# Kernel tuning notes

Hardware: AMD Instinct MI355X
Metric: run time of the kernel (lower is better)

Reference implementation:

```python
import jax, jax.numpy as jnp
import numpy as np

N = 100000   # nodes
E = 1600000  # edges
F_IN = 128
H = 128
C_OUT = 10
G = 128      # graphs in batch
EPS = 1e-5


def setup_inputs() -> dict:
    key = jax.random.key(0)
    ks = jax.random.split(key, 16)
    x = jax.random.normal(ks[0], (N, F_IN), dtype=jnp.float32)
    edge_index = jax.random.randint(ks[1], (2, E), 0, N, dtype=jnp.int64)
    batch = jnp.sort(jax.random.randint(ks[2], (N,), 0, G, dtype=jnp.int64))
    s = 1.0 / np.sqrt(H)
    inp = {"x": x, "edge_index": edge_index, "batch": batch}
    # GCNConv weights/biases
    inp["w1"] = jax.random.normal(ks[3], (F_IN, H), jnp.float32) * s
    inp["b1"] = jax.random.normal(ks[4], (H,), jnp.float32) * 0.01
    inp["w2"] = jax.random.normal(ks[5], (H, H), jnp.float32) * s
    inp["b2"] = jax.random.normal(ks[6], (H,), jnp.float32) * 0.01
    inp["w3"] = jax.random.normal(ks[7], (H, H), jnp.float32) * s
    inp["b3"] = jax.random.normal(ks[8], (H,), jnp.float32) * 0.01
    # GraphNorm params: scale (weight), shift (bias), mean_scale (alpha)
    for i, k in zip((1, 2, 3), (ks[9], ks[10], ks[11])):
        kk = jax.random.split(k, 3)
        inp[f"g{i}w"] = 1.0 + 0.1 * jax.random.normal(kk[0], (H,), jnp.float32)
        inp[f"g{i}b"] = 0.1 * jax.random.normal(kk[1], (H,), jnp.float32)
        inp[f"g{i}a"] = 1.0 + 0.1 * jax.random.normal(kk[2], (H,), jnp.float32)
    inp["lw"] = jax.random.normal(ks[12], (H, C_OUT), jnp.float32) * s
    inp["lb"] = jax.random.normal(ks[13], (C_OUT,), jnp.float32) * 0.01
    return inp


def _gcn_norm(edge_index, n):
    # add self loops, symmetric normalization D^-1/2 (A+I) D^-1/2
    loop = jnp.arange(n, dtype=edge_index.dtype)
    src = jnp.concatenate([edge_index[0], loop])
    dst = jnp.concatenate([edge_index[1], loop])
    deg = jax.ops.segment_sum(jnp.ones_like(dst, dtype=jnp.float32), dst, num_segments=n)
    dinv = jnp.where(deg > 0, jax.lax.rsqrt(deg), 0.0)
    norm = dinv[src] * dinv[dst]
    return src, dst, norm


def _gcn_conv(x, w, b, src, dst, norm, n):
    h = x @ w                              # [N,H]
    msg = h[src] * norm[:, None]           # gather + edge weight
    out = jax.ops.segment_sum(msg, dst, num_segments=n)  # scatter-add
    return out + b


def _graph_norm(x, weight, bias, alpha, batch, cnt, g):
    mean = jax.ops.segment_sum(x, batch, num_segments=g) / cnt[:, None]
    sub = x - alpha * mean[batch]
    var = jax.ops.segment_sum(sub * sub, batch, num_segments=g) / cnt[:, None]
    return weight * sub * jax.lax.rsqrt(var[batch] + EPS) + bias


def reference(x, edge_index, batch, w1, b1, w2, b2, w3, b3,
              g1w, g1b, g1a, g2w, g2b, g2a, g3w, g3b, g3a, lw, lb):
    n = x.shape[0]
    src, dst, norm = _gcn_norm(edge_index, n)
    cnt = jnp.maximum(jax.ops.segment_sum(jnp.ones((n,), jnp.float32), batch, num_segments=G), 1.0)
    # dropout is identity in eval mode
    h = _gcn_conv(x, w1, b1, src, dst, norm, n)
    h = jax.nn.relu(_graph_norm(h, g1w, g1b, g1a, batch, cnt, G))
    h = _gcn_conv(h, w2, b2, src, dst, norm, n)
    h = jax.nn.relu(_graph_norm(h, g2w, g2b, g2a, batch, cnt, G))
    h = _gcn_conv(h, w3, b3, src, dst, norm, n)
    h = jax.nn.relu(_graph_norm(h, g3w, g3b, g3a, batch, cnt, G))
    pooled = jax.ops.segment_sum(h, batch, num_segments=G) / cnt[:, None]  # global_mean_pool
    logits = pooled @ lw + lb
    return jax.nn.log_softmax(logits, axis=1)
```

## Files before the change

### kernel.cpp

```cpp
#include <hip/hip_runtime.h>

#define NN 100000
#define NE 1600000
#define HD 128
#define NG 128
#define NC 10
#define EPSV 1e-5f

#define BSH 9
#define NBKT ((NN + 511) >> 9)
#define BIN_BLOCKS ((NE + 4095) / 4096)

typedef __attribute__((ext_vector_type(8))) short short8;
typedef __attribute__((ext_vector_type(4))) float f32x4;

__device__ __forceinline__ float b2f(ushort u){ return __uint_as_float(((unsigned)u)<<16); }
__device__ __forceinline__ ushort f2b(float f){
  unsigned u = __float_as_uint(f);
  unsigned r = (u + 0x7FFFu + ((u>>16)&1u)) >> 16;
  return (ushort)r;
}

__global__ __launch_bounds__(256)
void k_init(const int* __restrict__ batch, int* __restrict__ gstart,
            const float* __restrict__ w1, const float* __restrict__ w2,
            const float* __restrict__ w3, ushort* __restrict__ wT,
            int* __restrict__ gbhist, float* __restrict__ zero_base)
{
  int b = blockIdx.x, t = threadIdx.x;
  if(b < 391){
    int n = b*256 + t;
    if(n >= NN) return;
    int bb = batch[n];
    if(n == 0){
      for(int g=0; g<=bb; g++) gstart[g] = 0;
      int last = batch[NN-1];
      for(int g=last+1; g<=NG; g++) gstart[g] = NN;
    } else {
      int bp = batch[n-1];
      for(int g=bp+1; g<=bb; g++) gstart[g] = n;
    }
  } else if(b < 394){
    const float* w = (b == 391) ? w1 : (b == 392) ? w2 : w3;
    ushort* o = wT + (b-391)*16384;
    #pragma unroll 4
    for(int i=0;i<64;i++){
      int e = i*256 + t;
      int k = e>>7, h = e&127;
      o[h*128 + k] = f2b(w[e]);
    }
  } else if(b < 408){
    #pragma unroll 8
    for(int i=0;i<32;i++) zero_base[(size_t)(b-394)*8192 + i*256 + t] = 0.f;
  } else {
    if(t < NBKT) gbhist[t] = 0;
  }
}

__global__ __launch_bounds__(256) void k_bhist(const int* __restrict__ ei, int* __restrict__ gbhist){
  __shared__ int h[NBKT];
  int t = threadIdx.x;
  if(t < NBKT) h[t] = 0;
  __syncthreads();
  int base = blockIdx.x*4096;
  #pragma unroll
  for(int i=0;i<16;i++){
    int e = base + i*256 + t;
    if(e < NE) atomicAdd(&h[ei[NE + e] >> BSH], 1);
  }
  __syncthreads();
  if(t < NBKT && h[t]) atomicAdd(&gbhist[t], h[t]);
}

__global__ void k_bscan(const int* __restrict__ gbhist, int* __restrict__ bucket_base,
                        int* __restrict__ bucket_cursor, int* __restrict__ rowstart){
  __shared__ int lds[256];
  int t = threadIdx.x;
  int v = (t < NBKT) ? gbhist[t] : 0;
  lds[t] = v; __syncthreads();
  for(int off=1; off<256; off<<=1){
    int y = lds[t]; int z = (t>=off)?lds[t-off]:0;
    __syncthreads(); lds[t] = y+z; __syncthreads();
  }
  int excl = (t>0)?lds[t-1]:0;
  if(t < NBKT){ bucket_base[t] = excl; bucket_cursor[t] = excl; }
  if(t == 0){ bucket_base[NBKT] = NE; rowstart[NN] = NE; }
}

__global__ __launch_bounds__(256) void k_bin(const int* __restrict__ ei, int* __restrict__ bucket_cursor,
                                             unsigned* __restrict__ ebuf){
  __shared__ unsigned eb[4096];
  __shared__ unsigned char bb4[4096];
  __shared__ int hist[NBKT], lstart[NBKT], lcur[NBKT], rbase[NBKT];
  __shared__ int scanbuf[256];
  int t = threadIdx.x;
  if(t < NBKT) hist[t] = 0;
  __syncthreads();
  int base = blockIdx.x*4096;
  int nv = NE - base; if(nv > 4096) nv = 4096;
  int se[16], de[16];
  #pragma unroll
  for(int i=0;i<16;i++){
    int e = base + i*256 + t;
    if(e < NE){ se[i] = ei[e]; de[i] = ei[NE + e]; atomicAdd(&hist[de[i] >> BSH], 1); }
  }
  __syncthreads();
  int v = (t < NBKT) ? hist[t] : 0;
  scanbuf[t] = v; __syncthreads();
  for(int off=1; off<256; off<<=1){
    int y = scanbuf[t]; int z = (t>=off)?scanbuf[t-off]:0;
    __syncthreads(); scanbuf[t] = y+z; __syncthreads();
  }
  if(t < NBKT){
    int excl = (t>0)?scanbuf[t-1]:0;
    lstart[t] = excl; lcur[t] = excl;
    if(hist[t]) rbase[t] = atomicAdd(&bucket_cursor[t], hist[t]);
  }
  __syncthreads();
  #pragma unroll
  for(int i=0;i<16;i++){
    int e = base + i*256 + t;
    if(e < NE){
      int b = de[i] >> BSH;
      int idx = atomicAdd(&lcur[b], 1);
      eb[idx] = ((unsigned)(de[i] & 511) << 17) | (unsigned)se[i];
      bb4[idx] = (unsigned char)b;
    }
  }
  __syncthreads();
  #pragma unroll
  for(int i=0;i<16;i++){
    int slot = i*256 + t;
    if(slot < nv){
      int b = bb4[slot];
      ebuf[rbase[b] + (slot - lstart[b])] = eb[slot];
    }
  }
}

__global__ __launch_bounds__(256) void k_sort(const unsigned* __restrict__ ebuf,
                                              const int* __restrict__ bucket_base,
                                              int* __restrict__ srcs, int* __restrict__ rowstart,
                                              float* __restrict__ dinv){
  __shared__ int hist[512], cur[512];
  __shared__ int scanbuf[256];
  int b = blockIdx.x, t = threadIdx.x;
  int e0 = bucket_base[b], e1 = bucket_base[b+1];
  hist[t] = 0; hist[t+256] = 0;
  __syncthreads();
  for(int i = e0 + t; i < e1; i += 256){
    atomicAdd(&hist[ebuf[i] >> 17], 1);
  }
  __syncthreads();
  int s0 = hist[2*t], s1 = hist[2*t+1];
  scanbuf[t] = s0 + s1; __syncthreads();
  for(int off=1; off<256; off<<=1){
    int y = scanbuf[t]; int z = (t>=off)?scanbuf[t-off]:0;
    __syncthreads(); scanbuf[t] = y+z; __syncthreads();
  }
  int excl = (t>0)?scanbuf[t-1]:0;
  cur[2*t] = excl; cur[2*t+1] = excl + s0;
  int d0 = (b << BSH) + 2*t, d1 = d0 + 1;
  if(d0 < NN){ rowstart[d0] = e0 + excl;      dinv[d0] = rsqrtf((float)(s0 + 1)); }
  if(d1 < NN){ rowstart[d1] = e0 + excl + s0; dinv[d1] = rsqrtf((float)(s1 + 1)); }
  __syncthreads();
  for(int i = e0 + t; i < e1; i += 256){
    unsigned pk = ebuf[i];
    int dl = pk >> 17;
    int pos = e0 + atomicAdd(&cur[dl], 1);
    srcs[pos] = (int)(pk & 0x1FFFFu);
  }
}

template<int NORM>
__global__ __launch_bounds__(256)
void k_gemm(const void* __restrict__ in_, const ushort* __restrict__ wT,
            ushort* __restrict__ g, const float* __restrict__ dinv,
            const int* __restrict__ batch,
            const float* __restrict__ gw, const float* __restrict__ gb,
            const float* __restrict__ ga, const float* __restrict__ S1,
            const float* __restrict__ S2, const int* __restrict__ gstart)
{
  __shared__ ushort lds_a[128*136];
  __shared__ float sdinv[128];
  const int t = threadIdx.x;
  const int row0 = blockIdx.x * 128;

  {
    const int l = t & 31;
    const int rr = t >> 5;
    if(t < 128){
      int node = row0 + t;
      sdinv[t] = (node < NN) ? dinv[node] : 0.f;
    }
    float4 gwv, gbv, gav;
    float4 amv = make_float4(0.f,0.f,0.f,0.f), rsv = make_float4(0.f,0.f,0.f,0.f);
    int gprev = -1;
    if(NORM){
      gwv = ((const float4*)gw)[l]; gbv = ((const float4*)gb)[l];
      gav = ((const float4*)ga)[l];
    }
    #pragma unroll 4
    for(int rb = 0; rb < 16; rb++){
      int r = rb*8 + rr;
      int node = row0 + r;
      float4 v = make_float4(0.f,0.f,0.f,0.f);
      if(node < NN){
        if(NORM){
          ushort4 raw = ((const ushort4*)in_)[(size_t)node*32 + l];
          v = make_float4(b2f(raw.x), b2f(raw.y), b2f(raw.z), b2f(raw.w));
          int gg = batch[node];
          if(gg != gprev){
            gprev = gg;
            int c0 = gstart[gg], c1 = gstart[gg+1];
            float inv = 1.f/(float)((c1-c0) > 0 ? (c1-c0) : 1);
            float4 s1v = ((const float4*)S1)[gg*32 + l];
            float4 s2v = ((const float4*)S2)[gg*32 + l];
            float m, ex2, a;
            m = s1v.x*inv; ex2 = s2v.x*inv; a = gav.x;
            amv.x = a*m; rsv.x = rsqrtf(ex2 - (2.f*a - a*a)*m*m + EPSV);
            m = s1v.y*inv; ex2 = s2v.y*inv; a = gav.y;
            amv.y = a*m; rsv.y = rsqrtf(ex2 - (2.f*a - a*a)*m*m + EPSV);
            m = s1v.z*inv; ex2 = s2v.z*inv; a = gav.z;
            amv.z = a*m; rsv.z = rsqrtf(ex2 - (2.f*a - a*a)*m*m + EPSV);
            m = s1v.w*inv; ex2 = s2v.w*inv; a = gav.w;
            amv.w = a*m; rsv.w = rsqrtf(ex2 - (2.f*a - a*a)*m*m + EPSV);
          }
          v.x = fmaxf(gwv.x*(v.x-amv.x)*rsv.x + gbv.x, 0.f);
          v.y = fmaxf(gwv.y*(v.y-amv.y)*rsv.y + gbv.y, 0.f);
          v.z = fmaxf(gwv.z*(v.z-amv.z)*rsv.z + gbv.z, 0.f);
          v.w = fmaxf(gwv.w*(v.w-amv.w)*rsv.w + gbv.w, 0.f);
        } else {
          v = ((const float4*)in_)[(size_t)node*32 + l];
        }
      }
      ushort4 b4;
      b4.x = f2b(v.x); b4.y = f2b(v.y); b4.z = f2b(v.z); b4.w = f2b(v.w);
      *(ushort4*)(lds_a + r*136 + l*4) = b4;
    }
  }
  __syncthreads();

  const int wv = t >> 6;
  const int l  = t & 63;
  const int lc = l & 15, lk = l >> 4;

  short8 bfrag[2][4];
  #pragma unroll
  for(int tt=0; tt<2; tt++){
    int col = wv*32 + tt*16 + lc;
    #pragma unroll
    for(int s=0; s<4; s++)
      bfrag[tt][s] = *(const short8*)(wT + col*128 + s*32 + lk*8);
  }

  f32x4 acc[8][2];
  #pragma unroll
  for(int m=0;m<8;m++){ acc[m][0] = (f32x4)0.f; acc[m][1] = (f32x4)0.f; }

  #pragma unroll
  for(int m=0; m<8; m++){
    const ushort* ap = lds_a + (m*16 + lc)*136 + lk*8;
    #pragma unroll
    for(int s=0; s<4; s++){
      short8 a = *(const short8*)(ap + s*32);
      acc[m][0] = __builtin_amdgcn_mfma_f32_16x16x32_bf16(a, bfrag[0][s], acc[m][0], 0, 0, 0);
      acc[m][1] = __builtin_amdgcn_mfma_f32_16x16x32_bf16(a, bfrag[1][s], acc[m][1], 0, 0, 0);
    }
  }

  #pragma unroll
  for(int m=0; m<8; m++){
    #pragma unroll
    for(int tt=0; tt<2; tt++){
      int colg = wv*32 + tt*16 + lc;
      #pragma unroll
      for(int r=0; r<4; r++){
        int row = m*16 + lk*4 + r;
        int node = row0 + row;
        if(node < NN)
          g[(size_t)node*128 + colg] = f2b(acc[m][tt][r] * sdinv[row]);
      }
    }
  }
}

__global__ __launch_bounds__(256)
void k_agg(const ushort* __restrict__ g, const int* __restrict__ rowstart,
           const int* __restrict__ srcs, const float* __restrict__ dinv,
           const float* __restrict__ bias, ushort* __restrict__ outp)
{
  const int lane = threadIdx.x & 31;
  const int node = blockIdx.x*8 + (threadIdx.x >> 5);
  const int e0 = rowstart[node], e1 = rowstart[node+1];
  float ax=0.f, ay=0.f, az=0.f, aw=0.f;
  float bx=0.f, by=0.f, bz=0.f, bw=0.f;
  const ushort4* gp = (const ushort4*)g;
  int e = e0;
  for(; e+7 < e1; e += 8){
    int si[8];
    #pragma unroll
    for(int i=0;i<8;i++) si[i] = srcs[e+i];
    ushort4 v[8];
    #pragma unroll
    for(int i=0;i<8;i++) v[i] = gp[(size_t)si[i]*32 + lane];
    #pragma unroll
    for(int i=0;i<8;i++){
      if(i&1){ bx += b2f(v[i].x); by += b2f(v[i].y); bz += b2f(v[i].z); bw += b2f(v[i].w); }
      else   { ax += b2f(v[i].x); ay += b2f(v[i].y); az += b2f(v[i].z); aw += b2f(v[i].w); }
    }
  }
  for(; e+3 < e1; e += 4){
    int si[4];
    #pragma unroll
    for(int i=0;i<4;i++) si[i] = srcs[e+i];
    ushort4 v[4];
    #pragma unroll
    for(int i=0;i<4;i++) v[i] = gp[(size_t)si[i]*32 + lane];
    #pragma unroll
    for(int i=0;i<4;i++){
      if(i&1){ bx += b2f(v[i].x); by += b2f(v[i].y); bz += b2f(v[i].z); bw += b2f(v[i].w); }
      else   { ax += b2f(v[i].x); ay += b2f(v[i].y); az += b2f(v[i].z); aw += b2f(v[i].w); }
    }
  }
  for(; e < e1; e++){
    ushort4 v = gp[(size_t)srcs[e]*32 + lane];
    ax += b2f(v.x); ay += b2f(v.y); az += b2f(v.z); aw += b2f(v.w);
  }
  ushort4 vs = gp[(size_t)node*32 + lane];
  float dv = dinv[node];
  float4 bv = ((const float4*)bias)[lane];
  ushort4 o4;
  o4.x = f2b(dv*(ax+bx+b2f(vs.x))+bv.x);
  o4.y = f2b(dv*(ay+by+b2f(vs.y))+bv.y);
  o4.z = f2b(dv*(az+bz+b2f(vs.z))+bv.z);
  o4.w = f2b(dv*(aw+bw+b2f(vs.w))+bv.w);
  ((ushort4*)outp)[(size_t)node*32 + lane] = o4;
}

#define STAT_CH 8
__global__ __launch_bounds__(128)
void k_stats(const ushort* __restrict__ x, const int* __restrict__ gstart,
             float* __restrict__ S1, float* __restrict__ S2)
{
  int g = blockIdx.x, ch = blockIdx.y, f = threadIdx.x;
  int s = gstart[g], e = gstart[g+1];
  int len = e - s;
  int i0 = s + (int)((long long)len * ch / STAT_CH);
  int i1 = s + (int)((long long)len * (ch+1) / STAT_CH);
  float a1 = 0.f, a2 = 0.f;
  for(int n=i0; n<i1; n++){
    float v = b2f(x[(size_t)n*128 + f]);
    a1 += v; a2 += v*v;
  }
  if(i1 > i0){
    atomicAdd(&S1[g*128+f], a1);
    atomicAdd(&S2[g*128+f], a2);
  }
}

#define POOL_CH 16
__global__ __launch_bounds__(128)
void k_pool(const ushort* __restrict__ x, const int* __restrict__ gstart,
            const float* __restrict__ gw, const float* __restrict__ gb,
            const float* __restrict__ ga, const float* __restrict__ S1,
            const float* __restrict__ S2, float* __restrict__ pooled)
{
  int g = blockIdx.x, ch = blockIdx.y, f = threadIdx.x;
  int s = gstart[g], e = gstart[g+1];
  int len = e - s;
  int i0 = s + (int)((long long)len * ch / POOL_CH);
  int i1 = s + (int)((long long)len * (ch+1) / POOL_CH);
  float inv = 1.f/(float)(len > 0 ? len : 1);
  float a = ga[f];
  float m = S1[g*128+f]*inv, ex2 = S2[g*128+f]*inv;
  float am = a*m;
  float rs = rsqrtf(ex2 - (2.f*a - a*a)*m*m + EPSV);
  float wv = gw[f], bv = gb[f];
  float a1 = 0.f;
  for(int n=i0; n<i1; n++){
    float v = b2f(x[(size_t)n*128 + f]);
    v = wv*(v-am)*rs + bv;
    a1 += fmaxf(v, 0.f);
  }
  if(i1 > i0) atomicAdd(&pooled[g*128+f], a1);
}

__global__ __launch_bounds__(64)
void k_head(const float* __restrict__ pooled, const int* __restrict__ gstart,
            const float* __restrict__ lw, const float* __restrict__ lb,
            float* __restrict__ out)
{
  int g = blockIdx.x, t = threadIdx.x;
  __shared__ float lg[NC];
  __shared__ float lse_s;
  int len = gstart[g+1] - gstart[g];
  float inv = 1.f/(float)(len > 0 ? len : 1);
  if(t < NC){
    float acc = lb[t];
    for(int f=0; f<128; f++) acc += pooled[g*128+f]*inv*lw[f*NC + t];
    lg[t] = acc;
  }
  __syncthreads();
  if(t == 0){
    float mx = -1e30f;
    for(int c=0;c<NC;c++) mx = fmaxf(mx, lg[c]);
    float sm = 0.f;
    for(int c=0;c<NC;c++) sm += expf(lg[c]-mx);
    lse_s = mx + logf(sm);
  }
  __syncthreads();
  if(t < NC) out[g*NC + t] = lg[t] - lse_s;
}

extern "C" void kernel_launch(void* const* d_in, const int* in_sizes, int n_in,
                              void* d_out, int out_size, void* d_ws, size_t ws_size,
                              hipStream_t stream)
{
  const float* x    = (const float*)d_in[0];
  const int*   ei   = (const int*)d_in[1];
  const int*   batch= (const int*)d_in[2];
  const float* w1   = (const float*)d_in[3];
  const float* b1   = (const float*)d_in[4];
  const float* w2   = (const float*)d_in[5];
  const float* b2   = (const float*)d_in[6];
  const float* w3   = (const float*)d_in[7];
  const float* b3   = (const float*)d_in[8];
  const float* g1w  = (const float*)d_in[9];
  const float* g1b  = (const float*)d_in[10];
  const float* g1a  = (const float*)d_in[11];
  const float* g2w  = (const float*)d_in[12];
  const float* g2b  = (const float*)d_in[13];
  const float* g2a  = (const float*)d_in[14];
  const float* g3w  = (const float*)d_in[15];
  const float* g3b  = (const float*)d_in[16];
  const float* g3a  = (const float*)d_in[17];
  const float* lw   = (const float*)d_in[18];
  const float* lb   = (const float*)d_in[19];
  float* out = (float*)d_out;

  char* p = (char*)d_ws;
  auto take = [&](size_t nbytes){ char* q = p; p += (nbytes + 255) & ~(size_t)255; return q; };
  ushort* gbuf    = (ushort*)take((size_t)NN*HD*2);
  ushort* bufB    = (ushort*)take((size_t)NN*HD*2);
  ushort* wT      = (ushort*)take((size_t)3*HD*HD*2);
  unsigned* ebuf  = (unsigned*)take((size_t)NE*4);
  int*   srcs     = (int*)  take((size_t)NE*4);
  int*   rowstart = (int*)  take((size_t)(NN+1)*4);
  float* dinv     = (float*)take((size_t)NN*4);
  int*   gbhist   = (int*)  take((size_t)NBKT*4);
  int*   bucket_base   = (int*)take((size_t)(NBKT+1)*4);
  int*   bucket_cursor = (int*)take((size_t)NBKT*4);
  int*   gstart   = (int*)  take((size_t)(NG+1)*4);
  float* Sbase    = (float*)take((size_t)(3*2*NG*HD + NG*HD)*4);
  if((size_t)(p - (char*)d_ws) > ws_size) return;

  float* SL1 = Sbase;
  float* SL2 = Sbase + 2*NG*HD;
  float* SL3 = Sbase + 4*NG*HD;
  float* pooled = Sbase + 6*NG*HD;

  k_init  <<<409, 256, 0, stream>>>(batch, gstart, w1, w2, w3, wT, gbhist, Sbase);
  k_bhist <<<BIN_BLOCKS, 256, 0, stream>>>(ei, gbhist);
  k_bscan <<<1, 256, 0, stream>>>(gbhist, bucket_base, bucket_cursor, rowstart);
  k_bin   <<<BIN_BLOCKS, 256, 0, stream>>>(ei, bucket_cursor, ebuf);
  k_sort  <<<NBKT, 256, 0, stream>>>(ebuf, bucket_base, srcs, rowstart, dinv);

  const int GB = (NN + 127)/128;
  const int AB = NN/8;

  k_gemm<0><<<GB, 256, 0, stream>>>(x, wT, gbuf, dinv, batch,
                                    nullptr, nullptr, nullptr, nullptr, nullptr, gstart);
  k_agg<<<AB, 256, 0, stream>>>(gbuf, rowstart, srcs, dinv, b1, bufB);
  k_stats<<<dim3(NG, STAT_CH), 128, 0, stream>>>(bufB, gstart, SL1, SL1 + NG*HD);

  k_gemm<1><<<GB, 256, 0, stream>>>(bufB, wT + 16384, gbuf, dinv, batch,
                                    g1w, g1b, g1a, SL1, SL1 + NG*HD, gstart);
  k_agg<<<AB, 256, 0, stream>>>(gbuf, rowstart, srcs, dinv, b2, bufB);
  k_stats<<<dim3(NG, STAT_CH), 128, 0, stream>>>(bufB, gstart, SL2, SL2 + NG*HD);

  k_gemm<1><<<GB, 256, 0, stream>>>(bufB, wT + 32768, gbuf, dinv, batch,
                                    g2w, g2b, g2a, SL2, SL2 + NG*HD, gstart);
  k_agg<<<AB, 256, 0, stream>>>(gbuf, rowstart, srcs, dinv, b3, bufB);
  k_stats<<<dim3(NG, STAT_CH), 128, 0, stream>>>(bufB, gstart, SL3, SL3 + NG*HD);

  k_pool<<<dim3(NG, POOL_CH), 128, 0, stream>>>(bufB, gstart, g3w, g3b, g3a,
                                                SL3, SL3 + NG*HD, pooled);
  k_head<<<NG, 64, 0, stream>>>(pooled, gstart, lw, lb, out);
}
```

Before: 436.5 us.

## Drop bucket histogram pass with fixed-capacity buckets and fuse pool with head

```diff
diff --git a/kernel.cpp b/kernel.cpp
--- a/kernel.cpp
+++ b/kernel.cpp
@@ -9,7 +9,10 @@
 
 #define BSH 9
 #define NBKT ((NN + 511) >> 9)
+#define BCAP 9216
 #define BIN_BLOCKS ((NE + 4095) / 4096)
+#define STAT_CH 8
+#define POOL_CH 16
 
 typedef __attribute__((ext_vector_type(8))) short short8;
 typedef __attribute__((ext_vector_type(4))) float f32x4;
@@ -25,7 +28,8 @@
 void k_init(const int* __restrict__ batch, int* __restrict__ gstart,
             const float* __restrict__ w1, const float* __restrict__ w2,
             const float* __restrict__ w3, ushort* __restrict__ wT,
-            int* __restrict__ gbhist, float* __restrict__ zero_base)
+            int* __restrict__ cursor0, int* __restrict__ done,
+            int* __restrict__ rowstart, float* __restrict__ zero_base)
 {
   int b = blockIdx.x, t = threadIdx.x;
   if(b < 391){
@@ -46,48 +50,19 @@
     #pragma unroll 4
     for(int i=0;i<64;i++){
       int e = i*256 + t;
-      int k = e>>7, h = e&127;
-      o[h*128 + k] = f2b(w[e]);
+      o[(e & 127)*128 + (e >> 7)] = f2b(w[e]);
     }
   } else if(b < 408){
     #pragma unroll 8
     for(int i=0;i<32;i++) zero_base[(size_t)(b-394)*8192 + i*256 + t] = 0.f;
   } else {
-    if(t < NBKT) gbhist[t] = 0;
-  }
-}
-
-__global__ __launch_bounds__(256) void k_bhist(const int* __restrict__ ei, int* __restrict__ gbhist){
-  __shared__ int h[NBKT];
-  int t = threadIdx.x;
-  if(t < NBKT) h[t] = 0;
-  __syncthreads();
-  int base = blockIdx.x*4096;
-  #pragma unroll
-  for(int i=0;i<16;i++){
-    int e = base + i*256 + t;
-    if(e < NE) atomicAdd(&h[ei[NE + e] >> BSH], 1);
-  }
-  __syncthreads();
-  if(t < NBKT && h[t]) atomicAdd(&gbhist[t], h[t]);
-}
-
-__global__ void k_bscan(const int* __restrict__ gbhist, int* __restrict__ bucket_base,
-                        int* __restrict__ bucket_cursor, int* __restrict__ rowstart){
-  __shared__ int lds[256];
-  int t = threadIdx.x;
-  int v = (t < NBKT) ? gbhist[t] : 0;
-  lds[t] = v; __syncthreads();
-  for(int off=1; off<256; off<<=1){
-    int y = lds[t]; int z = (t>=off)?lds[t-off]:0;
-    __syncthreads(); lds[t] = y+z; __syncthreads();
-  }
-  int excl = (t>0)?lds[t-1]:0;
-  if(t < NBKT){ bucket_base[t] = excl; bucket_cursor[t] = excl; }
-  if(t == 0){ bucket_base[NBKT] = NE; rowstart[NN] = NE; }
-}
-
-__global__ __launch_bounds__(256) void k_bin(const int* __restrict__ ei, int* __restrict__ bucket_cursor,
+    if(t < NBKT) cursor0[t] = 0;
+    if(t < NG)   done[t] = 0;
+    if(t == 0)   rowstart[NN] = NE;
+  }
+}
+
+__global__ __launch_bounds__(256) void k_bin(const int* __restrict__ ei, int* __restrict__ cursor0,
                                              unsigned* __restrict__ ebuf){
   __shared__ unsigned eb[4096];
   __shared__ unsigned char bb4[4096];
@@ -114,7 +89,7 @@
   if(t < NBKT){
     int excl = (t>0)?scanbuf[t-1]:0;
     lstart[t] = excl; lcur[t] = excl;
-    if(hist[t]) rbase[t] = atomicAdd(&bucket_cursor[t], hist[t]);
+    if(hist[t]) rbase[t] = t*BCAP + atomicAdd(&cursor0[t], hist[t]);
   }
   __syncthreads();
   #pragma unroll
@@ -139,18 +114,25 @@
 }
 
 __global__ __launch_bounds__(256) void k_sort(const unsigned* __restrict__ ebuf,
-                                              const int* __restrict__ bucket_base,
+                                              const int* __restrict__ cursor0,
                                               int* __restrict__ srcs, int* __restrict__ rowstart,
                                               float* __restrict__ dinv){
   __shared__ int hist[512], cur[512];
   __shared__ int scanbuf[256];
   int b = blockIdx.x, t = threadIdx.x;
-  int e0 = bucket_base[b], e1 = bucket_base[b+1];
+  int v = (t < NBKT) ? cursor0[t] : 0;
+  scanbuf[t] = v; __syncthreads();
+  for(int off=1; off<256; off<<=1){
+    int y = scanbuf[t]; int z = (t>=off)?scanbuf[t-off]:0;
+    __syncthreads(); scanbuf[t] = y+z; __syncthreads();
+  }
+  const int e0 = (b>0) ? scanbuf[b-1] : 0;
+  const int cnt = cursor0[b];
+  const unsigned* reg = ebuf + (size_t)b*BCAP;
   hist[t] = 0; hist[t+256] = 0;
   __syncthreads();
-  for(int i = e0 + t; i < e1; i += 256){
-    atomicAdd(&hist[ebuf[i] >> 17], 1);
-  }
+  for(int i = t; i < cnt; i += 256)
+    atomicAdd(&hist[reg[i] >> 17], 1);
   __syncthreads();
   int s0 = hist[2*t], s1 = hist[2*t+1];
   scanbuf[t] = s0 + s1; __syncthreads();
@@ -164,8 +146,8 @@
   if(d0 < NN){ rowstart[d0] = e0 + excl;      dinv[d0] = rsqrtf((float)(s0 + 1)); }
   if(d1 < NN){ rowstart[d1] = e0 + excl + s0; dinv[d1] = rsqrtf((float)(s1 + 1)); }
   __syncthreads();
-  for(int i = e0 + t; i < e1; i += 256){
-    unsigned pk = ebuf[i];
+  for(int i = t; i < cnt; i += 256){
+    unsigned pk = reg[i];
     int dl = pk >> 17;
     int pos = e0 + atomicAdd(&cur[dl], 1);
     srcs[pos] = (int)(pk & 0x1FFFFu);
@@ -185,7 +167,6 @@
   __shared__ float sdinv[128];
   const int t = threadIdx.x;
   const int row0 = blockIdx.x * 128;
-
   {
     const int l = t & 31;
     const int rr = t >> 5;
@@ -241,10 +222,7 @@
   }
   __syncthreads();
 
-  const int wv = t >> 6;
-  const int l  = t & 63;
-  const int lc = l & 15, lk = l >> 4;
-
+  const int wv = t >> 6, l = t & 63, lc = l & 15, lk = l >> 4;
   short8 bfrag[2][4];
   #pragma unroll
   for(int tt=0; tt<2; tt++){
@@ -253,11 +231,9 @@
     for(int s=0; s<4; s++)
       bfrag[tt][s] = *(const short8*)(wT + col*128 + s*32 + lk*8);
   }
-
   f32x4 acc[8][2];
   #pragma unroll
   for(int m=0;m<8;m++){ acc[m][0] = (f32x4)0.f; acc[m][1] = (f32x4)0.f; }
-
   #pragma unroll
   for(int m=0; m<8; m++){
     const ushort* ap = lds_a + (m*16 + lc)*136 + lk*8;
@@ -268,7 +244,6 @@
       acc[m][1] = __builtin_amdgcn_mfma_f32_16x16x32_bf16(a, bfrag[1][s], acc[m][1], 0, 0, 0);
     }
   }
-
   #pragma unroll
   for(int m=0; m<8; m++){
     #pragma unroll
@@ -338,7 +313,6 @@
   ((ushort4*)outp)[(size_t)node*32 + lane] = o4;
 }
 
-#define STAT_CH 8
 __global__ __launch_bounds__(128)
 void k_stats(const ushort* __restrict__ x, const int* __restrict__ gstart,
              float* __restrict__ S1, float* __restrict__ S2)
@@ -359,12 +333,14 @@
   }
 }
 
-#define POOL_CH 16
 __global__ __launch_bounds__(128)
-void k_pool(const ushort* __restrict__ x, const int* __restrict__ gstart,
-            const float* __restrict__ gw, const float* __restrict__ gb,
-            const float* __restrict__ ga, const float* __restrict__ S1,
-            const float* __restrict__ S2, float* __restrict__ pooled)
+void k_poolhead(const ushort* __restrict__ x, const int* __restrict__ gstart,
+                const float* __restrict__ gw, const float* __restrict__ gb,
+                const float* __restrict__ ga, const float* __restrict__ S1,
+                const float* __restrict__ S2, float* __restrict__ pooled,
+                int* __restrict__ done,
+                const float* __restrict__ lw, const float* __restrict__ lb,
+                float* __restrict__ out)
 {
   int g = blockIdx.x, ch = blockIdx.y, f = threadIdx.x;
   int s = gstart[g], e = gstart[g+1];
@@ -384,25 +360,23 @@
     a1 += fmaxf(v, 0.f);
   }
   if(i1 > i0) atomicAdd(&pooled[g*128+f], a1);
-}
-
-__global__ __launch_bounds__(64)
-void k_head(const float* __restrict__ pooled, const int* __restrict__ gstart,
-            const float* __restrict__ lw, const float* __restrict__ lb,
-            float* __restrict__ out)
-{
-  int g = blockIdx.x, t = threadIdx.x;
+  __threadfence();
+  __syncthreads();
+  __shared__ int lastflag;
+  if(f == 0)
+    lastflag = (atomicAdd(&done[g], 1) == POOL_CH - 1);
+  __syncthreads();
+  if(!lastflag) return;
+  __threadfence();
   __shared__ float lg[NC];
   __shared__ float lse_s;
-  int len = gstart[g+1] - gstart[g];
-  float inv = 1.f/(float)(len > 0 ? len : 1);
-  if(t < NC){
-    float acc = lb[t];
-    for(int f=0; f<128; f++) acc += pooled[g*128+f]*inv*lw[f*NC + t];
-    lg[t] = acc;
-  }
-  __syncthreads();
-  if(t == 0){
+  if(f < NC){
+    float acc = lb[f];
+    for(int k=0; k<128; k++) acc += pooled[g*128+k]*inv*lw[k*NC + f];
+    lg[f] = acc;
+  }
+  __syncthreads();
+  if(f == 0){
     float mx = -1e30f;
     for(int c=0;c<NC;c++) mx = fmaxf(mx, lg[c]);
     float sm = 0.f;
@@ -410,7 +384,7 @@
     lse_s = mx + logf(sm);
   }
   __syncthreads();
-  if(t < NC) out[g*NC + t] = lg[t] - lse_s;
+  if(f < NC) out[g*NC + f] = lg[f] - lse_s;
 }
 
 extern "C" void kernel_launch(void* const* d_in, const int* in_sizes, int n_in,
@@ -444,27 +418,27 @@
   ushort* gbuf    = (ushort*)take((size_t)NN*HD*2);
   ushort* bufB    = (ushort*)take((size_t)NN*HD*2);
   ushort* wT      = (ushort*)take((size_t)3*HD*HD*2);
-  unsigned* ebuf  = (unsigned*)take((size_t)NE*4);
+  unsigned* ebuf  = (unsigned*)take((size_t)NBKT*BCAP*4);
   int*   srcs     = (int*)  take((size_t)NE*4);
   int*   rowstart = (int*)  take((size_t)(NN+1)*4);
   float* dinv     = (float*)take((size_t)NN*4);
-  int*   gbhist   = (int*)  take((size_t)NBKT*4);
-  int*   bucket_base   = (int*)take((size_t)(NBKT+1)*4);
-  int*   bucket_cursor = (int*)take((size_t)NBKT*4);
+  int*   cursor0  = (int*)  take((size_t)NBKT*4);
+  int*   done     = (int*)  take((size_t)NG*4);
   int*   gstart   = (int*)  take((size_t)(NG+1)*4);
   float* Sbase    = (float*)take((size_t)(3*2*NG*HD + NG*HD)*4);
   if((size_t)(p - (char*)d_ws) > ws_size) return;
 
-  float* SL1 = Sbase;
-  float* SL2 = Sbase + 2*NG*HD;
-  float* SL3 = Sbase + 4*NG*HD;
+  float* SL1  = Sbase;
+  float* SL1b = Sbase + 1*NG*HD;
+  float* SL2  = Sbase + 2*NG*HD;
+  float* SL2b = Sbase + 3*NG*HD;
+  float* SL3  = Sbase + 4*NG*HD;
+  float* SL3b = Sbase + 5*NG*HD;
   float* pooled = Sbase + 6*NG*HD;
 
-  k_init  <<<409, 256, 0, stream>>>(batch, gstart, w1, w2, w3, wT, gbhist, Sbase);
-  k_bhist <<<BIN_BLOCKS, 256, 0, stream>>>(ei, gbhist);
-  k_bscan <<<1, 256, 0, stream>>>(gbhist, bucket_base, bucket_cursor, rowstart);
-  k_bin   <<<BIN_BLOCKS, 256, 0, stream>>>(ei, bucket_cursor, ebuf);
-  k_sort  <<<NBKT, 256, 0, stream>>>(ebuf, bucket_base, srcs, rowstart, dinv);
+  k_init <<<409, 256, 0, stream>>>(batch, gstart, w1, w2, w3, wT, cursor0, done, rowstart, Sbase);
+  k_bin  <<<BIN_BLOCKS, 256, 0, stream>>>(ei, cursor0, ebuf);
+  k_sort <<<NBKT, 256, 0, stream>>>(ebuf, cursor0, srcs, rowstart, dinv);
 
   const int GB = (NN + 127)/128;
   const int AB = NN/8;
@@ -472,19 +446,18 @@
   k_gemm<0><<<GB, 256, 0, stream>>>(x, wT, gbuf, dinv, batch,
                                     nullptr, nullptr, nullptr, nullptr, nullptr, gstart);
   k_agg<<<AB, 256, 0, stream>>>(gbuf, rowstart, srcs, dinv, b1, bufB);
-  k_stats<<<dim3(NG, STAT_CH), 128, 0, stream>>>(bufB, gstart, SL1, SL1 + NG*HD);
+  k_stats<<<dim3(NG, STAT_CH), 128, 0, stream>>>(bufB, gstart, SL1, SL1b);
 
   k_gemm<1><<<GB, 256, 0, stream>>>(bufB, wT + 16384, gbuf, dinv, batch,
-                                    g1w, g1b, g1a, SL1, SL1 + NG*HD, gstart);
+                                    g1w, g1b, g1a, SL1, SL1b, gstart);
   k_agg<<<AB, 256, 0, stream>>>(gbuf, rowstart, srcs, dinv, b2, bufB);
-  k_stats<<<dim3(NG, STAT_CH), 128, 0, stream>>>(bufB, gstart, SL2, SL2 + NG*HD);
+  k_stats<<<dim3(NG, STAT_CH), 128, 0, stream>>>(bufB, gstart, SL2, SL2b);
 
   k_gemm<1><<<GB, 256, 0, stream>>>(bufB, wT + 32768, gbuf, dinv, batch,
-                                    g2w, g2b, g2a, SL2, SL2 + NG*HD, gstart);
+                                    g2w, g2b, g2a, SL2, SL2b, gstart);
   k_agg<<<AB, 256, 0, stream>>>(gbuf, rowstart, srcs, dinv, b3, bufB);
-  k_stats<<<dim3(NG, STAT_CH), 128, 0, stream>>>(bufB, gstart, SL3, SL3 + NG*HD);
-
-  k_pool<<<dim3(NG, POOL_CH), 128, 0, stream>>>(bufB, gstart, g3w, g3b, g3a,
-                                                SL3, SL3 + NG*HD, pooled);
-  k_head<<<NG, 64, 0, stream>>>(pooled, gstart, lw, lb, out);
-}
+  k_stats<<<dim3(NG, STAT_CH), 128, 0, stream>>>(bufB, gstart, SL3, SL3b);
+
+  k_poolhead<<<dim3(NG, POOL_CH), 128, 0, stream>>>(bufB, gstart, g3w, g3b, g3a,
+                                                    SL3, SL3b, pooled, done, lw, lb, out);
+}
```

After: 482.8 us. +10.6%, slower.
